# Kernel tuning notes

Measured on AMD Instinct MI355X. Metric: run time of the kernel, lower is better.

## Reference

```python
import jax, jax.numpy as jnp
import numpy as np

N_NODES = 50000
N_EDGES = 400000
IN, HID, OUT = 256, 64, 64
HEADS = (8, 8, 1)
NEG_SLOPE = 0.2


def setup_inputs() -> dict:
    key = jax.random.key(0)
    ks = jax.random.split(key, 16)
    def lin(k, fi, fo):
        return jax.random.normal(k, (fi, fo), jnp.float32) / np.sqrt(fi)
    H0, H1, H2 = HEADS
    return {
        "x": jax.random.normal(ks[0], (N_NODES, IN), jnp.float32),
        "src": jax.random.randint(ks[1], (N_EDGES,), 0, N_NODES),
        "dst": jax.random.randint(ks[2], (N_EDGES,), 0, N_NODES),
        # layer 0: in=256 -> (8 heads, 64)
        "W1": lin(ks[3], IN, H0 * HID),
        "al1": 0.1 * jax.random.normal(ks[4], (H0, HID), jnp.float32),
        "ar1": 0.1 * jax.random.normal(ks[5], (H0, HID), jnp.float32),
        "b1": jnp.zeros((H0 * HID,), jnp.float32),
        # layer 1: in=512 -> (8 heads, 64), identity residual (512 == 8*64)
        "W2": lin(ks[6], H0 * HID, H1 * HID),
        "al2": 0.1 * jax.random.normal(ks[7], (H1, HID), jnp.float32),
        "ar2": 0.1 * jax.random.normal(ks[8], (H1, HID), jnp.float32),
        "b2": jnp.zeros((H1 * HID,), jnp.float32),
        # layer 2: in=512 -> (1 head, 64), linear residual projection
        "W3": lin(ks[9], H1 * HID, H2 * OUT),
        "al3": 0.1 * jax.random.normal(ks[10], (H2, OUT), jnp.float32),
        "ar3": 0.1 * jax.random.normal(ks[11], (H2, OUT), jnp.float32),
        "b3": jnp.zeros((H2 * OUT,), jnp.float32),
        "Wr3": lin(ks[12], H1 * HID, H2 * OUT),
    }


def _gat_conv(h, src, dst, W, al, ar, b, res, act):
    # DGL GATConv on a homogeneous graph (feat_src == feat_dst).
    N = h.shape[0]
    H, D = al.shape
    f = (h @ W).reshape(N, H, D)                       # [N,H,D]
    el = jnp.sum(f * al[None], axis=-1)                # [N,H]
    er = jnp.sum(f * ar[None], axis=-1)                # [N,H]
    e = jax.nn.leaky_relu(el[src] + er[dst], NEG_SLOPE)  # [E,H]
    # segment softmax over incoming edges of each dst node
    m = jax.ops.segment_max(e, dst, num_segments=N)    # [N,H]
    ex = jnp.exp(e - m[dst])
    denom = jax.ops.segment_sum(ex, dst, num_segments=N)
    alpha = ex / denom[dst]                            # [E,H]
    msg = f[src] * alpha[:, :, None]                   # [E,H,D]
    rst = jax.ops.segment_sum(msg, dst, num_segments=N)  # [N,H,D]
    if res is not None:
        rst = rst + res
    rst = rst + b.reshape(1, H, D)
    return act(rst) if act is not None else rst


def reference(x, src, dst, W1, al1, ar1, b1, W2, al2, ar2, b2,
              W3, al3, ar3, b3, Wr3):
    N = x.shape[0]
    h = _gat_conv(x, src, dst, W1, al1, ar1, b1, None, jax.nn.elu)
    h = h.reshape(N, -1)                               # flatten(1)
    res2 = h.reshape(N, HEADS[1], HID)                 # identity residual
    h = _gat_conv(h, src, dst, W2, al2, ar2, b2, res2, jax.nn.elu)
    h = h.reshape(N, -1)
    res3 = (h @ Wr3).reshape(N, HEADS[2], OUT)         # projected residual
    h = _gat_conv(h, src, dst, W3, al3, ar3, b3, res3, None)
    return h.mean(axis=1)                              # mean over heads
```

## Files before the change

kernel.cpp:

```cpp
#include <hip/hip_runtime.h>
#include <hip/hip_bf16.h>

#define N_NODES 50000
#define M_PAD 50048
#define N_EDGES 400000
#define SCAN_B 256

typedef __attribute__((ext_vector_type(8))) short short8;
typedef __attribute__((ext_vector_type(4))) float f32x4;

__device__ __forceinline__ float b2f(unsigned short u) {
    return __uint_as_float(((unsigned)u) << 16);
}
__device__ __forceinline__ unsigned short f2b(float f) {
    unsigned u = __float_as_uint(f);
    return (unsigned short)((u + 0x7fffu + ((u >> 16) & 1u)) >> 16);
}
__device__ __forceinline__ float blo(unsigned u) { return __uint_as_float(u << 16); }
__device__ __forceinline__ float bhi(unsigned u) { return __uint_as_float(u & 0xffff0000u); }

__device__ __forceinline__ void gload_lds16(const void* g, void* l) {
    __builtin_amdgcn_global_load_lds(
        (const __attribute__((address_space(1))) unsigned int*)g,
        (__attribute__((address_space(3))) unsigned int*)l, 16, 0, 0);
}

__global__ __launch_bounds__(256) void conv_x4(const float* __restrict__ x,
                                               unsigned short* __restrict__ xb, int n4) {
    int i = blockIdx.x * blockDim.x + threadIdx.x;
    if (i >= n4) return;
    float4 v = *(const float4*)&x[(size_t)i * 4];
    unsigned short o[4] = {f2b(v.x), f2b(v.y), f2b(v.z), f2b(v.w)};
    *(ushort2*)&xb[(size_t)i * 4] = make_ushort2(o[0], o[1]);
    *(ushort2*)&xb[(size_t)i * 4 + 2] = make_ushort2(o[2], o[3]);
}

__global__ __launch_bounds__(256) void conv_wt(const float* __restrict__ W,
                                               unsigned short* __restrict__ Wt,
                                               int K, int N) {
    int o = blockIdx.x * blockDim.x + threadIdx.x;
    if (o >= K * N) return;
    int n = o / K, k = o % K;
    Wt[o] = f2b(W[(size_t)k * N + n]);
}

__global__ __launch_bounds__(256, 2) void gemm_mfma(const unsigned short* __restrict__ A,
                                                    const unsigned short* __restrict__ Bt,
                                                    unsigned short* __restrict__ C,
                                                    int M, int N, int K) {
    __shared__ unsigned short As[128 * 32];
    __shared__ unsigned short Bs[128 * 32];
    const int tid = threadIdx.x;
    const int w = tid >> 6, l = tid & 63;
    const int bm = blockIdx.y * 128, bn = blockIdx.x * 128;
    const int wr = w >> 1, wc = w & 1;
    const int rA = l >> 2;
    const int kA = (l & 3) * 8;
    const int fr = l & 15, fq = l >> 4;
    f32x4 acc[4][4] = {};

    for (int k0 = 0; k0 < K; k0 += 32) {
#pragma unroll
        for (int j = 0; j < 2; ++j) {
            int row = w * 32 + j * 16 + rA;
            gload_lds16(&A[(size_t)(bm + row) * K + k0 + kA], &As[(w * 2 + j) * 512]);
            gload_lds16(&Bt[(size_t)(bn + row) * K + k0 + kA], &Bs[(w * 2 + j) * 512]);
        }
        __syncthreads();
        short8 a[4], b[4];
#pragma unroll
        for (int m = 0; m < 4; ++m)
            a[m] = *(const short8*)&As[(wr * 64 + m * 16 + fr) * 32 + fq * 8];
#pragma unroll
        for (int n = 0; n < 4; ++n)
            b[n] = *(const short8*)&Bs[(wc * 64 + n * 16 + fr) * 32 + fq * 8];
#pragma unroll
        for (int m = 0; m < 4; ++m)
#pragma unroll
            for (int n = 0; n < 4; ++n)
                acc[m][n] = __builtin_amdgcn_mfma_f32_16x16x32_bf16(a[m], b[n], acc[m][n], 0, 0, 0);
        __syncthreads();
    }

#pragma unroll
    for (int m = 0; m < 4; ++m) {
#pragma unroll
        for (int j = 0; j < 4; ++j) {
            int r = bm + wr * 64 + m * 16 + fq * 4 + j;
            if (r < M) {
#pragma unroll
                for (int n = 0; n < 4; ++n)
                    C[(size_t)r * N + bn + wc * 64 + n * 16 + fr] = f2b(acc[m][n][j]);
            }
        }
    }
}

__global__ __launch_bounds__(256) void eler8_k(const unsigned short* __restrict__ f,
                                               const float* __restrict__ al,
                                               const float* __restrict__ ar,
                                               float* __restrict__ el,
                                               float* __restrict__ er, int N) {
    int w = (blockIdx.x * blockDim.x + threadIdx.x) >> 6;
    int lane = threadIdx.x & 63;
    if (w >= N) return;
    const int h = lane >> 3, sl = (lane & 7) * 8;
    uint4 pk = *(const uint4*)&f[(size_t)w * 512 + h * 64 + sl];
    float4 a0 = *(const float4*)&al[h * 64 + sl];
    float4 a1 = *(const float4*)&al[h * 64 + sl + 4];
    float4 r0 = *(const float4*)&ar[h * 64 + sl];
    float4 r1 = *(const float4*)&ar[h * 64 + sl + 4];
    float x0 = blo(pk.x), x1 = bhi(pk.x), x2 = blo(pk.y), x3 = bhi(pk.y);
    float x4 = blo(pk.z), x5 = bhi(pk.z), x6 = blo(pk.w), x7 = bhi(pk.w);
    float pl = x0 * a0.x + x1 * a0.y + x2 * a0.z + x3 * a0.w +
               x4 * a1.x + x5 * a1.y + x6 * a1.z + x7 * a1.w;
    float pr = x0 * r0.x + x1 * r0.y + x2 * r0.z + x3 * r0.w +
               x4 * r1.x + x5 * r1.y + x6 * r1.z + x7 * r1.w;
#pragma unroll
    for (int off = 1; off < 8; off <<= 1) {
        pl += __shfl_xor(pl, off);
        pr += __shfl_xor(pr, off);
    }
    if ((lane & 7) == 0) {
        el[(size_t)w * 8 + h] = pl;
        er[(size_t)w * 8 + h] = pr;
    }
}

__global__ __launch_bounds__(256) void eler1_k(const unsigned short* __restrict__ f, int ldf,
                                               const float* __restrict__ al,
                                               const float* __restrict__ ar,
                                               float* __restrict__ el,
                                               float* __restrict__ er, int N) {
    int gw = (blockIdx.x * blockDim.x + threadIdx.x) >> 6;
    int lane = threadIdx.x & 63;
    if (gw >= N) return;
    float v = b2f(f[(size_t)gw * ldf + lane]);
    float pl = v * al[lane];
    float pr = v * ar[lane];
#pragma unroll
    for (int off = 32; off; off >>= 1) {
        pl += __shfl_xor(pl, off);
        pr += __shfl_xor(pr, off);
    }
    if (lane == 0) {
        el[gw] = pl;
        er[gw] = pr;
    }
}

__global__ __launch_bounds__(256) void hist_k(const int* __restrict__ dst,
                                              int* __restrict__ deg, int E) {
    int i = blockIdx.x * blockDim.x + threadIdx.x;
    if (i < E) atomicAdd(&deg[dst[i]], 1);
}

__global__ __launch_bounds__(SCAN_B) void scan_blocks(const int* __restrict__ in,
                                                      int* __restrict__ out,
                                                      int* __restrict__ part, int n) {
    __shared__ int tmp[SCAN_B];
    int t = threadIdx.x, g = blockIdx.x * SCAN_B + t;
    int v = (g < n) ? in[g] : 0;
    tmp[t] = v;
    __syncthreads();
    for (int off = 1; off < SCAN_B; off <<= 1) {
        int add = (t >= off) ? tmp[t - off] : 0;
        __syncthreads();
        tmp[t] += add;
        __syncthreads();
    }
    if (g < n) out[g] = tmp[t] - v;
    if (t == SCAN_B - 1) part[blockIdx.x] = tmp[t];
}

__global__ __launch_bounds__(SCAN_B) void scan_part(int* __restrict__ part, int n) {
    __shared__ int tmp[SCAN_B];
    int t = threadIdx.x;
    int v = (t < n) ? part[t] : 0;
    tmp[t] = v;
    __syncthreads();
    for (int off = 1; off < SCAN_B; off <<= 1) {
        int add = (t >= off) ? tmp[t - off] : 0;
        __syncthreads();
        tmp[t] += add;
        __syncthreads();
    }
    if (t < n) part[t] = tmp[t] - v;
}

__global__ __launch_bounds__(256) void add_off(int* __restrict__ rowptr,
                                               int* __restrict__ cursor,
                                               const int* __restrict__ part,
                                               int n, int E) {
    int g = blockIdx.x * blockDim.x + threadIdx.x;
    if (g < n) {
        int v = rowptr[g] + part[g / SCAN_B];
        rowptr[g] = v;
        cursor[g] = v;
    }
    if (g == 0) rowptr[n] = E;
}

__global__ __launch_bounds__(256) void scatter_k(const int* __restrict__ src,
                                                 const int* __restrict__ dst,
                                                 int* __restrict__ cursor,
                                                 int* __restrict__ csr_src, int E) {
    int e = blockIdx.x * blockDim.x + threadIdx.x;
    if (e < E) {
        int p = atomicAdd(&cursor[dst[e]], 1);
        csr_src[p] = src[e];
    }
}

template <bool HAS_INIT>
__global__ __launch_bounds__(256) void gat_agg8(const unsigned short* __restrict__ f,
                                                const float* __restrict__ el,
                                                const float* __restrict__ er,
                                                const int* __restrict__ rowptr,
                                                const int* __restrict__ csr_src,
                                                const unsigned short* __restrict__ init,
                                                const float* __restrict__ bias,
                                                unsigned short* __restrict__ outb, int N) {
    int w = (blockIdx.x * blockDim.x + threadIdx.x) >> 6;
    int lane = threadIdx.x & 63;
    if (w >= N) return;
    const int d = w;
    const int s0 = rowptr[d], s1 = rowptr[d + 1];
    const int hh = lane & 7;
    const float erh = er[(size_t)d * 8 + hh];

    float mx = -1e30f;
    for (int i = s0 + (lane >> 3); i < s1; i += 8) {
        float v = el[(size_t)csr_src[i] * 8 + hh] + erh;
        v = v > 0.f ? v : 0.2f * v;
        mx = fmaxf(mx, v);
    }
#pragma unroll
    for (int off = 8; off < 64; off <<= 1) mx = fmaxf(mx, __shfl_xor(mx, off));

    float sm = 0.f;
    for (int i = s0 + (lane >> 3); i < s1; i += 8) {
        float v = el[(size_t)csr_src[i] * 8 + hh] + erh;
        v = v > 0.f ? v : 0.2f * v;
        sm += __expf(v - mx);
    }
#pragma unroll
    for (int off = 8; off < 64; off <<= 1) sm += __shfl_xor(sm, off);
    const float inv = sm > 0.f ? 1.0f / sm : 0.f;

    const int myhead = lane >> 3;
    const int sl = (lane & 7) * 8;
    float acc[8] = {};
    for (int i = s0; i < s1; ++i) {
        int sn = csr_src[i];
        float v = el[(size_t)sn * 8 + hh] + erh;
        v = v > 0.f ? v : 0.2f * v;
        float am = __expf(v - mx) * inv;
        float alpha = __shfl(am, myhead);
        uint4 pk = *(const uint4*)&f[(size_t)sn * 512 + myhead * 64 + sl];
        acc[0] += blo(pk.x) * alpha;
        acc[1] += bhi(pk.x) * alpha;
        acc[2] += blo(pk.y) * alpha;
        acc[3] += bhi(pk.y) * alpha;
        acc[4] += blo(pk.z) * alpha;
        acc[5] += bhi(pk.z) * alpha;
        acc[6] += blo(pk.w) * alpha;
        acc[7] += bhi(pk.w) * alpha;
    }

    float4 b0 = *(const float4*)&bias[myhead * 64 + sl];
    float4 b1 = *(const float4*)&bias[myhead * 64 + sl + 4];
    float bb[8] = {b0.x, b0.y, b0.z, b0.w, b1.x, b1.y, b1.z, b1.w};
    if (HAS_INIT) {
        uint4 iv = *(const uint4*)&init[(size_t)d * 512 + myhead * 64 + sl];
        acc[0] += blo(iv.x); acc[1] += bhi(iv.x);
        acc[2] += blo(iv.y); acc[3] += bhi(iv.y);
        acc[4] += blo(iv.z); acc[5] += bhi(iv.z);
        acc[6] += blo(iv.w); acc[7] += bhi(iv.w);
    }
    unsigned short ob[8];
#pragma unroll
    for (int j = 0; j < 8; ++j) {
        float v = acc[j] + bb[j];
        v = v > 0.f ? v : __expf(v) - 1.f;
        ob[j] = f2b(v);
    }
    uint4 ov;
    ov.x = (unsigned)ob[0] | ((unsigned)ob[1] << 16);
    ov.y = (unsigned)ob[2] | ((unsigned)ob[3] << 16);
    ov.z = (unsigned)ob[4] | ((unsigned)ob[5] << 16);
    ov.w = (unsigned)ob[6] | ((unsigned)ob[7] << 16);
    *(uint4*)&outb[((size_t)d * 8 + myhead) * 64 + sl] = ov;
}

__global__ __launch_bounds__(256) void gat_agg1(const unsigned short* __restrict__ f,
                                                const float* __restrict__ el,
                                                const float* __restrict__ er,
                                                const int* __restrict__ rowptr,
                                                const int* __restrict__ csr_src,
                                                const float* __restrict__ bias,
                                                float* __restrict__ outf, int N) {
    int w = (blockIdx.x * blockDim.x + threadIdx.x) >> 6;
    int lane = threadIdx.x & 63;
    if (w >= N) return;
    const int d = w;
    const int s0 = rowptr[d], s1 = rowptr[d + 1];
    const float erh = er[d];

    float mx = -1e30f;
    for (int i = s0 + lane; i < s1; i += 64) {
        float v = el[csr_src[i]] + erh;
        v = v > 0.f ? v : 0.2f * v;
        mx = fmaxf(mx, v);
    }
#pragma unroll
    for (int off = 1; off < 64; off <<= 1) mx = fmaxf(mx, __shfl_xor(mx, off));

    float sm = 0.f;
    for (int i = s0 + lane; i < s1; i += 64) {
        float v = el[csr_src[i]] + erh;
        v = v > 0.f ? v : 0.2f * v;
        sm += __expf(v - mx);
    }
#pragma unroll
    for (int off = 1; off < 64; off <<= 1) sm += __shfl_xor(sm, off);
    const float inv = sm > 0.f ? 1.0f / sm : 0.f;

    const int esub = lane >> 3, sl = (lane & 7) * 8;
    float acc[8] = {};
    for (int i0 = s0; i0 < s1; i0 += 8) {
        int i = i0 + esub;
        bool valid = i < s1;
        int sn = csr_src[valid ? i : s0];
        float v = el[sn] + erh;
        v = v > 0.f ? v : 0.2f * v;
        float alpha = valid ? __expf(v - mx) * inv : 0.f;
        uint4 pk = *(const uint4*)&f[(size_t)sn * 128 + sl];
        acc[0] += blo(pk.x) * alpha;
        acc[1] += bhi(pk.x) * alpha;
        acc[2] += blo(pk.y) * alpha;
        acc[3] += bhi(pk.y) * alpha;
        acc[4] += blo(pk.z) * alpha;
        acc[5] += bhi(pk.z) * alpha;
        acc[6] += blo(pk.w) * alpha;
        acc[7] += bhi(pk.w) * alpha;
    }
#pragma unroll
    for (int off = 8; off < 64; off <<= 1)
#pragma unroll
        for (int j = 0; j < 8; ++j) acc[j] += __shfl_xor(acc[j], off);

    if (esub == 0) {
        uint4 rv = *(const uint4*)&f[(size_t)d * 128 + 64 + sl];
        float rr[8] = {blo(rv.x), bhi(rv.x), blo(rv.y), bhi(rv.y),
                       blo(rv.z), bhi(rv.z), blo(rv.w), bhi(rv.w)};
#pragma unroll
        for (int j = 0; j < 8; ++j)
            outf[(size_t)d * 64 + sl + j] = acc[j] + bias[sl + j] + rr[j];
    }
}

extern "C" void kernel_launch(void* const* d_in, const int* in_sizes, int n_in,
                              void* d_out, int out_size, void* d_ws, size_t ws_size,
                              hipStream_t stream) {
    const float* x   = (const float*)d_in[0];
    const int*   src = (const int*)d_in[1];
    const int*   dst = (const int*)d_in[2];
    const float* W1  = (const float*)d_in[3];
    const float* al1 = (const float*)d_in[4];
    const float* ar1 = (const float*)d_in[5];
    const float* b1  = (const float*)d_in[6];
    const float* W2  = (const float*)d_in[7];
    const float* al2 = (const float*)d_in[8];
    const float* ar2 = (const float*)d_in[9];
    const float* b2  = (const float*)d_in[10];
    const float* W3  = (const float*)d_in[11];
    const float* al3 = (const float*)d_in[12];
    const float* ar3 = (const float*)d_in[13];
    const float* b3  = (const float*)d_in[14];
    const float* Wr3 = (const float*)d_in[15];
    float* out = (float*)d_out;

    unsigned short* xb   = (unsigned short*)d_ws;
    unsigned short* fb   = xb + (size_t)M_PAD * 256;
    unsigned short* h1b  = fb + (size_t)M_PAD * 512;
    unsigned short* h2b  = h1b + (size_t)M_PAD * 512;
    unsigned short* f3r  = h2b + (size_t)M_PAD * 512;
    unsigned short* Wt1  = f3r + (size_t)M_PAD * 128;
    unsigned short* Wt2  = Wt1 + 512 * 256;
    unsigned short* Wt3  = Wt2 + 512 * 512;
    float* el = (float*)(Wt3 + 128 * 512);
    float* er = el + (size_t)N_NODES * 8;
    int* rowptr  = (int*)(er + (size_t)N_NODES * 8);
    int* cursor  = rowptr + (N_NODES + 1);
    int* part    = cursor + N_NODES;
    int* csr_src = part + 256;

    const dim3 blk(256);
    const int E = N_EDGES, N = N_NODES;
    const int nb = (N + SCAN_B - 1) / SCAN_B;
    const int gy = (N + 127) / 128;

    conv_x4<<<(N * 64 + 255) / 256, blk, 0, stream>>>(x, xb, N * 64);
    conv_wt<<<(512 * 256 + 255) / 256, blk, 0, stream>>>(W1, Wt1, 256, 512);
    conv_wt<<<(512 * 512 + 255) / 256, blk, 0, stream>>>(W2, Wt2, 512, 512);
    conv_wt<<<(64 * 512 + 255) / 256, blk, 0, stream>>>(W3, Wt3, 512, 64);
    conv_wt<<<(64 * 512 + 255) / 256, blk, 0, stream>>>(Wr3, Wt3 + 64 * 512, 512, 64);

    hipMemsetAsync(cursor, 0, (size_t)N * 4, stream);
    hist_k<<<(E + 255) / 256, blk, 0, stream>>>(dst, cursor, E);
    scan_blocks<<<nb, SCAN_B, 0, stream>>>(cursor, rowptr, part, N);
    scan_part<<<1, SCAN_B, 0, stream>>>(part, nb);
    add_off<<<nb, blk, 0, stream>>>(rowptr, cursor, part, N, E);
    scatter_k<<<(E + 255) / 256, blk, 0, stream>>>(src, dst, cursor, csr_src, E);

    gemm_mfma<<<dim3(4, gy), blk, 0, stream>>>(xb, Wt1, fb, N, 512, 256);
    eler8_k<<<(N + 3) / 4, blk, 0, stream>>>(fb, al1, ar1, el, er, N);
    gat_agg8<false><<<(N + 3) / 4, blk, 0, stream>>>(
        fb, el, er, rowptr, csr_src, nullptr, b1, h1b, N);

    gemm_mfma<<<dim3(4, gy), blk, 0, stream>>>(h1b, Wt2, fb, N, 512, 512);
    eler8_k<<<(N + 3) / 4, blk, 0, stream>>>(fb, al2, ar2, el, er, N);
    gat_agg8<true><<<(N + 3) / 4, blk, 0, stream>>>(
        fb, el, er, rowptr, csr_src, h1b, b2, h2b, N);

    gemm_mfma<<<dim3(1, gy), blk, 0, stream>>>(h2b, Wt3, f3r, N, 128, 512);
    eler1_k<<<(N + 3) / 4, blk, 0, stream>>>(f3r, 128, al3, ar3, el, er, N);
    gat_agg1<<<(N + 3) / 4, blk, 0, stream>>>(
        f3r, el, er, rowptr, csr_src, b3, out, N);
}
```

Baseline: 395.2 us.

## Fuse attention logits into GEMM epilogue, merge weight conversions, batch edge gathers

Computes el/er (the per-head attention dot products) directly from the MFMA accumulators in the GEMM epilogue, which removes the separate eler kernels and their re-read of the feature matrix. The four weight transpose/convert launches are merged into one kernel. The 8-head aggregation now processes 8 edges per step: each lane loads a full 8-element slice of the 512-wide row and gets alpha and the source index via shuffles. This gives wider, more contiguous gathers per edge at the cost of extra shuffles and epilogue reductions. The el/er values are now computed from fp32 accumulators rather than from bf16-rounded features, which slightly changes numerics.

Measured after the change: 369.6 us. 1.07x faster.

```diff
diff --git a/kernel.cpp b/kernel.cpp
--- a/kernel.cpp
+++ b/kernel.cpp
@@ -35,19 +35,44 @@
     *(ushort2*)&xb[(size_t)i * 4 + 2] = make_ushort2(o[2], o[3]);
 }
 
-__global__ __launch_bounds__(256) void conv_wt(const float* __restrict__ W,
-                                               unsigned short* __restrict__ Wt,
-                                               int K, int N) {
+#define W1_SZ (512 * 256)
+#define W2_SZ (512 * 512)
+#define W3_SZ (64 * 512)
+__global__ __launch_bounds__(256) void conv_wt_all(const float* __restrict__ W1,
+                                                   const float* __restrict__ W2,
+                                                   const float* __restrict__ W3,
+                                                   const float* __restrict__ Wr3,
+                                                   unsigned short* __restrict__ Wt1,
+                                                   unsigned short* __restrict__ Wt2,
+                                                   unsigned short* __restrict__ Wt3) {
     int o = blockIdx.x * blockDim.x + threadIdx.x;
-    if (o >= K * N) return;
-    int n = o / K, k = o % K;
-    Wt[o] = f2b(W[(size_t)k * N + n]);
-}
-
+    if (o < W1_SZ) {
+        int n = o / 256, k = o % 256;
+        Wt1[o] = f2b(W1[(size_t)k * 512 + n]);
+    } else if (o < W1_SZ + W2_SZ) {
+        int oo = o - W1_SZ;
+        int n = oo / 512, k = oo % 512;
+        Wt2[oo] = f2b(W2[(size_t)k * 512 + n]);
+    } else if (o < W1_SZ + W2_SZ + W3_SZ) {
+        int oo = o - W1_SZ - W2_SZ;
+        int n = oo / 512, k = oo % 512;
+        Wt3[oo] = f2b(W3[(size_t)k * 64 + n]);
+    } else if (o < W1_SZ + W2_SZ + 2 * W3_SZ) {
+        int oo = o - W1_SZ - W2_SZ - W3_SZ;
+        int n = oo / 512, k = oo % 512;
+        Wt3[W3_SZ + oo] = f2b(Wr3[(size_t)k * 64 + n]);
+    }
+}
+
+template <int H, bool ELER>
 __global__ __launch_bounds__(256, 2) void gemm_mfma(const unsigned short* __restrict__ A,
                                                     const unsigned short* __restrict__ Bt,
                                                     unsigned short* __restrict__ C,
-                                                    int M, int N, int K) {
+                                                    const float* __restrict__ al,
+                                                    const float* __restrict__ ar,
+                                                    float* __restrict__ el,
+                                                    float* __restrict__ er,
+                                                    int M, int NN, int K) {
     __shared__ unsigned short As[128 * 32];
     __shared__ unsigned short Bs[128 * 32];
     const int tid = threadIdx.x;
@@ -82,6 +107,38 @@
         __syncthreads();
     }
 
+    if (ELER) {
+        const int head = (bn >> 6) + wc;
+        if (head < H) {
+            float alv[4], arv[4];
+#pragma unroll
+            for (int n = 0; n < 4; ++n) {
+                alv[n] = al[head * 64 + n * 16 + fr];
+                arv[n] = ar[head * 64 + n * 16 + fr];
+            }
+#pragma unroll
+            for (int m = 0; m < 4; ++m) {
+#pragma unroll
+                for (int j = 0; j < 4; ++j) {
+                    float pl = acc[m][0][j] * alv[0] + acc[m][1][j] * alv[1] +
+                               acc[m][2][j] * alv[2] + acc[m][3][j] * alv[3];
+                    float pr = acc[m][0][j] * arv[0] + acc[m][1][j] * arv[1] +
+                               acc[m][2][j] * arv[2] + acc[m][3][j] * arv[3];
+#pragma unroll
+                    for (int off = 1; off < 16; off <<= 1) {
+                        pl += __shfl_xor(pl, off);
+                        pr += __shfl_xor(pr, off);
+                    }
+                    int r = bm + wr * 64 + m * 16 + fq * 4 + j;
+                    if (fr == 0 && r < M) {
+                        el[(size_t)r * H + head] = pl;
+                        er[(size_t)r * H + head] = pr;
+                    }
+                }
+            }
+        }
+    }
+
 #pragma unroll
     for (int m = 0; m < 4; ++m) {
 #pragma unroll
@@ -90,62 +147,9 @@
             if (r < M) {
 #pragma unroll
                 for (int n = 0; n < 4; ++n)
-                    C[(size_t)r * N + bn + wc * 64 + n * 16 + fr] = f2b(acc[m][n][j]);
+                    C[(size_t)r * NN + bn + wc * 64 + n * 16 + fr] = f2b(acc[m][n][j]);
             }
         }
-    }
-}
-
-__global__ __launch_bounds__(256) void eler8_k(const unsigned short* __restrict__ f,
-                                               const float* __restrict__ al,
-                                               const float* __restrict__ ar,
-                                               float* __restrict__ el,
-                                               float* __restrict__ er, int N) {
-    int w = (blockIdx.x * blockDim.x + threadIdx.x) >> 6;
-    int lane = threadIdx.x & 63;
-    if (w >= N) return;
-    const int h = lane >> 3, sl = (lane & 7) * 8;
-    uint4 pk = *(const uint4*)&f[(size_t)w * 512 + h * 64 + sl];
-    float4 a0 = *(const float4*)&al[h * 64 + sl];
-    float4 a1 = *(const float4*)&al[h * 64 + sl + 4];
-    float4 r0 = *(const float4*)&ar[h * 64 + sl];
-    float4 r1 = *(const float4*)&ar[h * 64 + sl + 4];
-    float x0 = blo(pk.x), x1 = bhi(pk.x), x2 = blo(pk.y), x3 = bhi(pk.y);
-    float x4 = blo(pk.z), x5 = bhi(pk.z), x6 = blo(pk.w), x7 = bhi(pk.w);
-    float pl = x0 * a0.x + x1 * a0.y + x2 * a0.z + x3 * a0.w +
-               x4 * a1.x + x5 * a1.y + x6 * a1.z + x7 * a1.w;
-    float pr = x0 * r0.x + x1 * r0.y + x2 * r0.z + x3 * r0.w +
-               x4 * r1.x + x5 * r1.y + x6 * r1.z + x7 * r1.w;
-#pragma unroll
-    for (int off = 1; off < 8; off <<= 1) {
-        pl += __shfl_xor(pl, off);
-        pr += __shfl_xor(pr, off);
-    }
-    if ((lane & 7) == 0) {
-        el[(size_t)w * 8 + h] = pl;
-        er[(size_t)w * 8 + h] = pr;
-    }
-}
-
-__global__ __launch_bounds__(256) void eler1_k(const unsigned short* __restrict__ f, int ldf,
-                                               const float* __restrict__ al,
-                                               const float* __restrict__ ar,
-                                               float* __restrict__ el,
-                                               float* __restrict__ er, int N) {
-    int gw = (blockIdx.x * blockDim.x + threadIdx.x) >> 6;
-    int lane = threadIdx.x & 63;
-    if (gw >= N) return;
-    float v = b2f(f[(size_t)gw * ldf + lane]);
-    float pl = v * al[lane];
-    float pr = v * ar[lane];
-#pragma unroll
-    for (int off = 32; off; off >>= 1) {
-        pl += __shfl_xor(pl, off);
-        pr += __shfl_xor(pr, off);
-    }
-    if (lane == 0) {
-        el[gw] = pl;
-        er[gw] = pr;
     }
 }
 
@@ -227,10 +231,11 @@
     const int d = w;
     const int s0 = rowptr[d], s1 = rowptr[d + 1];
     const int hh = lane & 7;
+    const int esub = lane >> 3;
     const float erh = er[(size_t)d * 8 + hh];
 
     float mx = -1e30f;
-    for (int i = s0 + (lane >> 3); i < s1; i += 8) {
+    for (int i = s0 + esub; i < s1; i += 8) {
         float v = el[(size_t)csr_src[i] * 8 + hh] + erh;
         v = v > 0.f ? v : 0.2f * v;
         mx = fmaxf(mx, v);
@@ -239,7 +244,7 @@
     for (int off = 8; off < 64; off <<= 1) mx = fmaxf(mx, __shfl_xor(mx, off));
 
     float sm = 0.f;
-    for (int i = s0 + (lane >> 3); i < s1; i += 8) {
+    for (int i = s0 + esub; i < s1; i += 8) {
         float v = el[(size_t)csr_src[i] * 8 + hh] + erh;
         v = v > 0.f ? v : 0.2f * v;
         sm += __expf(v - mx);
@@ -249,30 +254,38 @@
     const float inv = sm > 0.f ? 1.0f / sm : 0.f;
 
     const int myhead = lane >> 3;
+    const int sl8 = lane * 8;
+    float acc[8] = {};
+    for (int i0 = s0; i0 < s1; i0 += 8) {
+        int i = i0 + esub;
+        bool valid = i < s1;
+        int sn_mine = csr_src[valid ? i : s0];
+        float v = el[(size_t)sn_mine * 8 + hh] + erh;
+        v = v > 0.f ? v : 0.2f * v;
+        float am = valid ? __expf(v - mx) * inv : 0.f;
+#pragma unroll
+        for (int j = 0; j < 8; ++j) {
+            if (i0 + j >= s1) break;
+            float alpha = __shfl(am, (j << 3) | myhead);
+            int sn = __shfl(sn_mine, j << 3);
+            uint4 pk = *(const uint4*)&f[(size_t)sn * 512 + sl8];
+            acc[0] += blo(pk.x) * alpha;
+            acc[1] += bhi(pk.x) * alpha;
+            acc[2] += blo(pk.y) * alpha;
+            acc[3] += bhi(pk.y) * alpha;
+            acc[4] += blo(pk.z) * alpha;
+            acc[5] += bhi(pk.z) * alpha;
+            acc[6] += blo(pk.w) * alpha;
+            acc[7] += bhi(pk.w) * alpha;
+        }
+    }
+
     const int sl = (lane & 7) * 8;
-    float acc[8] = {};
-    for (int i = s0; i < s1; ++i) {
-        int sn = csr_src[i];
-        float v = el[(size_t)sn * 8 + hh] + erh;
-        v = v > 0.f ? v : 0.2f * v;
-        float am = __expf(v - mx) * inv;
-        float alpha = __shfl(am, myhead);
-        uint4 pk = *(const uint4*)&f[(size_t)sn * 512 + myhead * 64 + sl];
-        acc[0] += blo(pk.x) * alpha;
-        acc[1] += bhi(pk.x) * alpha;
-        acc[2] += blo(pk.y) * alpha;
-        acc[3] += bhi(pk.y) * alpha;
-        acc[4] += blo(pk.z) * alpha;
-        acc[5] += bhi(pk.z) * alpha;
-        acc[6] += blo(pk.w) * alpha;
-        acc[7] += bhi(pk.w) * alpha;
-    }
-
     float4 b0 = *(const float4*)&bias[myhead * 64 + sl];
     float4 b1 = *(const float4*)&bias[myhead * 64 + sl + 4];
     float bb[8] = {b0.x, b0.y, b0.z, b0.w, b1.x, b1.y, b1.z, b1.w};
     if (HAS_INIT) {
-        uint4 iv = *(const uint4*)&init[(size_t)d * 512 + myhead * 64 + sl];
+        uint4 iv = *(const uint4*)&init[(size_t)d * 512 + sl8];
         acc[0] += blo(iv.x); acc[1] += bhi(iv.x);
         acc[2] += blo(iv.y); acc[3] += bhi(iv.y);
         acc[4] += blo(iv.z); acc[5] += bhi(iv.z);
@@ -290,7 +303,7 @@
     ov.y = (unsigned)ob[2] | ((unsigned)ob[3] << 16);
     ov.z = (unsigned)ob[4] | ((unsigned)ob[5] << 16);
     ov.w = (unsigned)ob[6] | ((unsigned)ob[7] << 16);
-    *(uint4*)&outb[((size_t)d * 8 + myhead) * 64 + sl] = ov;
+    *(uint4*)&outb[(size_t)d * 512 + sl8] = ov;
 }
 
 __global__ __launch_bounds__(256) void gat_agg1(const unsigned short* __restrict__ f,
@@ -402,10 +415,8 @@
     const int gy = (N + 127) / 128;
 
     conv_x4<<<(N * 64 + 255) / 256, blk, 0, stream>>>(x, xb, N * 64);
-    conv_wt<<<(512 * 256 + 255) / 256, blk, 0, stream>>>(W1, Wt1, 256, 512);
-    conv_wt<<<(512 * 512 + 255) / 256, blk, 0, stream>>>(W2, Wt2, 512, 512);
-    conv_wt<<<(64 * 512 + 255) / 256, blk, 0, stream>>>(W3, Wt3, 512, 64);
-    conv_wt<<<(64 * 512 + 255) / 256, blk, 0, stream>>>(Wr3, Wt3 + 64 * 512, 512, 64);
+    conv_wt_all<<<(W1_SZ + W2_SZ + 2 * W3_SZ + 255) / 256, blk, 0, stream>>>(
+        W1, W2, W3, Wr3, Wt1, Wt2, Wt3);
 
     hipMemsetAsync(cursor, 0, (size_t)N * 4, stream);
     hist_k<<<(E + 255) / 256, blk, 0, stream>>>(dst, cursor, E);
@@ -414,18 +425,18 @@
     add_off<<<nb, blk, 0, stream>>>(rowptr, cursor, part, N, E);
     scatter_k<<<(E + 255) / 256, blk, 0, stream>>>(src, dst, cursor, csr_src, E);
 
-    gemm_mfma<<<dim3(4, gy), blk, 0, stream>>>(xb, Wt1, fb, N, 512, 256);
-    eler8_k<<<(N + 3) / 4, blk, 0, stream>>>(fb, al1, ar1, el, er, N);
+    gemm_mfma<8, true><<<dim3(4, gy), blk, 0, stream>>>(
+        xb, Wt1, fb, al1, ar1, el, er, N, 512, 256);
     gat_agg8<false><<<(N + 3) / 4, blk, 0, stream>>>(
         fb, el, er, rowptr, csr_src, nullptr, b1, h1b, N);
 
-    gemm_mfma<<<dim3(4, gy), blk, 0, stream>>>(h1b, Wt2, fb, N, 512, 512);
-    eler8_k<<<(N + 3) / 4, blk, 0, stream>>>(fb, al2, ar2, el, er, N);
+    gemm_mfma<8, true><<<dim3(4, gy), blk, 0, stream>>>(
+        h1b, Wt2, fb, al2, ar2, el, er, N, 512, 512);
     gat_agg8<true><<<(N + 3) / 4, blk, 0, stream>>>(
         fb, el, er, rowptr, csr_src, h1b, b2, h2b, N);
 
-    gemm_mfma<<<dim3(1, gy), blk, 0, stream>>>(h2b, Wt3, f3r, N, 128, 512);
-    eler1_k<<<(N + 3) / 4, blk, 0, stream>>>(f3r, 128, al3, ar3, el, er, N);
+    gemm_mfma<1, true><<<dim3(1, gy), blk, 0, stream>>>(
+        h2b, Wt3, f3r, al3, ar3, el, er, N, 128, 512);
     gat_agg1<<<(N + 3) / 4, blk, 0, stream>>>(
         f3r, el, er, rowptr, csr_src, b3, out, N);
 }
```
